# Kernel optimization log

Hardware: AMD Instinct MI355X
Metric: run time of the kernel (lower is better)

The kernel has to match this reference:

```python
import jax, jax.numpy as jnp
import numpy as np

B, S, D, H = 8, 1024, 1024, 16  # batch, seq (queries==keys), d_model, heads
DH = D // H


def setup_inputs() -> dict:
    key = jax.random.key(0)
    ks = jax.random.split(key, 7)
    return {
        "query": jax.random.normal(ks[0], (B, S, D), dtype=jnp.float32),
        "key": jax.random.normal(ks[1], (B, S, D), dtype=jnp.float32),
        "value": jax.random.normal(ks[2], (B, S, D), dtype=jnp.float32),
        "valid_len": jax.random.randint(ks[3], (B, S), 0, S, dtype=jnp.int32),
        "Wq": jax.random.normal(ks[4], (D, D), dtype=jnp.float32) / np.sqrt(D),
        "Wk": jax.random.normal(ks[5], (D, D), dtype=jnp.float32) / np.sqrt(D),
        "Wv": jax.random.normal(ks[6], (D, D), dtype=jnp.float32) / np.sqrt(D),
    }


def reference(query, key, value, valid_len, Wq, Wk, Wv):
    b, sq, _ = query.shape
    sk = key.shape[1]
    # projections (bias-free Linear), then split hidden into H contiguous chunks per head
    q = (query @ Wq).reshape(b, sq, H, DH)  # [B,Sq,H,dh]
    k = (key @ Wk).reshape(b, sk, H, DH)
    v = (value @ Wv).reshape(b, sk, H, DH)
    scale = 1.0 / jnp.sqrt(jnp.asarray(DH, dtype=q.dtype))
    scores = jnp.einsum("bqhd,bkhd->bhqk", q, k) * scale  # [B,H,Sq,Sk]
    # per-query mask (valid_len.dim()==2 path): key index < valid_len[b, q]
    col = jnp.arange(sk)
    mask = col[None, None, None, :] < valid_len[:, None, :, None]  # [B,1,Sq,Sk]
    scores = jnp.where(mask, scores, jnp.asarray(-1000.0, dtype=scores.dtype))
    prob = jax.nn.softmax(scores, axis=-1)
    out = jnp.einsum("bhqk,bkhd->bqhd", prob, v)  # [B,Sq,H,dh]
    return out.reshape(b, sq, D)
```

## Files before the change

kernel.cpp:

```cpp
#include <hip/hip_runtime.h>
#include <hip/hip_bf16.h>
#include <stdint.h>


#define B_  8
#define S_  1024
#define D_  1024
#define H_  16
#define DH_ 64

typedef short bf16x8 __attribute__((ext_vector_type(8)));
typedef float f32x4  __attribute__((ext_vector_type(4)));
typedef unsigned short u16;
typedef uint32_t u32;
typedef u16 u16x8 __attribute__((ext_vector_type(8)));
typedef u16 u16x4 __attribute__((ext_vector_type(4)));

#define MASKVAL  (-1442.6950408889634f)
#define QSCALE   (0.18033688011112042f)

union U4 { u32 u[4]; bf16x8 v; };

__device__ __forceinline__ u16 f2bf(float f) {
    union { float f; uint32_t u; } v; v.f = f;
    uint32_t u = v.u;
    return (u16)((u + 0x7FFFu + ((u >> 16) & 1u)) >> 16);
}

__device__ __forceinline__ u32 cvtpk(float lo, float hi) {
    u32 r;
    asm("v_cvt_pk_bf16_f32 %0, %1, %2" : "=v"(r) : "v"(lo), "v"(hi));
    return r;
}

__device__ __forceinline__ void gload16(const void* g, const void* l) {
    __builtin_amdgcn_global_load_lds(
        (const __attribute__((address_space(1))) void*)g,
        (__attribute__((address_space(3))) void*)l, 16, 0, 0);
}

__global__ void transpose_w3_kernel(const float* __restrict__ Wq, const float* __restrict__ Wk,
                                    const float* __restrict__ Wv, u16* __restrict__ Wts) {
    __shared__ u16 tile[32 * 33];
    const int z = blockIdx.z;
    const float* W = (z == 0) ? Wq : (z == 1) ? Wk : Wv;
    u16* Wt = Wts + (size_t)z * D_ * D_;
    int k0 = blockIdx.y * 32, n0 = blockIdx.x * 32;
    int t = threadIdx.x;
    int c = t & 31;
    for (int p = 0; p < 4; ++p) {
        int r = p * 8 + (t >> 5);
        tile[r * 33 + c] = f2bf(W[(size_t)(k0 + r) * D_ + n0 + c]);
    }
    __syncthreads();
    int rn = t >> 3, c4 = t & 7;
    u16x4 v;
    for (int j = 0; j < 4; ++j) v[j] = tile[(c4 * 4 + j) * 33 + rn];
    *(u16x4*)(Wt + (size_t)(n0 + rn) * D_ + k0 + c4 * 4) = v;
}

__global__ __launch_bounds__(1024) void sort_vlen_kernel(const int* __restrict__ vlen,
                                                         int* __restrict__ qidx) {
    __shared__ u32 sk[1024];
    const int b = blockIdx.x, t = threadIdx.x;
    int k = vlen[b * S_ + t];
    u32 key = (k == 0) ? (u32)S_ : (u32)k;
    sk[t] = (key << 10) | (u32)t;
    __syncthreads();
    for (int sz = 2; sz <= 1024; sz <<= 1) {
        for (int st = sz >> 1; st > 0; st >>= 1) {
            int j = t ^ st;
            if (j > t) {
                u32 a = sk[t], c = sk[j];
                bool des = (t & sz) != 0;
                if ((a > c) != des) { sk[t] = c; sk[j] = a; }
            }
            __syncthreads();
        }
    }
    qidx[b * S_ + t] = (int)(sk[t] & 1023u);
}

__global__ __launch_bounds__(256) void gemm_qkv_kernel(const float* __restrict__ Aq,
                                                       const float* __restrict__ Ak,
                                                       const float* __restrict__ Av,
                                                       const u16* __restrict__ wts,
                                                       u16* __restrict__ qb, u16* __restrict__ kb,
                                                       u16* __restrict__ vb) {
    __shared__ float lds_a[2][128 * 32];
    __shared__ u16  lds_b[2][128 * 32];
    const int zy = blockIdx.y;
    const int z = zy >> 3;
    const float* A = (z == 0) ? Aq : (z == 1) ? Ak : Av;
    const u16* Bt = wts + (size_t)z * D_ * D_;
    u16* C = (z == 0) ? qb : (z == 1) ? kb : vb;
    const float cmul = (z == 0) ? QSCALE : 1.0f;

    const int t = threadIdx.x, w = t >> 6, l = t & 63;
    const int m0 = blockIdx.x * 128, n0 = (zy & 7) * 128;
    const int wr = w >> 1, wc = w & 1;
    const int l15 = l & 15, l4 = l >> 4;
    f32x4 acc[4][4] = {};

    auto stage = [&](int buf, int kt) {
        int k0 = kt * 32;
        #pragma unroll
        for (int i = 0; i < 4; ++i) {
            int c = i * 256 + t;
            int row = c >> 3, xs = (c & 7) ^ (row & 7);
            gload16(A + (size_t)(m0 + row) * D_ + k0 + xs * 4, &lds_a[buf][c * 4]);
        }
        #pragma unroll
        for (int i = 0; i < 2; ++i) {
            int c = i * 256 + t;
            int row = c >> 2, x = c & 3;
            gload16(Bt + (size_t)(n0 + row) * D_ + k0 + x * 8, &lds_b[buf][c * 8]);
        }
    };

    stage(0, 0);
    __syncthreads();
    int buf = 0;
    for (int kt = 0; kt < 32; ++kt) {
        if (kt + 1 < 32) stage(buf ^ 1, kt + 1);
        bf16x8 af[4], bfr[4];
        #pragma unroll
        for (int mi = 0; mi < 4; ++mi) {
            int r = wr * 64 + mi * 16 + l15;
            int c0 = (l4 * 2) ^ (r & 7), c1 = (l4 * 2 + 1) ^ (r & 7);
            float4 fa0 = *(const float4*)&lds_a[buf][r * 32 + c0 * 4];
            float4 fa1 = *(const float4*)&lds_a[buf][r * 32 + c1 * 4];
            U4 d;
            d.u[0] = cvtpk(fa0.x, fa0.y); d.u[1] = cvtpk(fa0.z, fa0.w);
            d.u[2] = cvtpk(fa1.x, fa1.y); d.u[3] = cvtpk(fa1.z, fa1.w);
            af[mi] = d.v;
        }
        #pragma unroll
        for (int ni = 0; ni < 4; ++ni)
            bfr[ni] = *(const bf16x8*)&lds_b[buf][(wc * 64 + ni * 16 + l15) * 32 + l4 * 8];
        #pragma unroll
        for (int mi = 0; mi < 4; ++mi)
            #pragma unroll
            for (int ni = 0; ni < 4; ++ni)
                acc[mi][ni] = __builtin_amdgcn_mfma_f32_16x16x32_bf16(af[mi], bfr[ni], acc[mi][ni], 0, 0, 0);
        __syncthreads();
        buf ^= 1;
    }
    #pragma unroll
    for (int mi = 0; mi < 4; ++mi)
        #pragma unroll
        for (int ni = 0; ni < 4; ++ni)
            #pragma unroll
            for (int r = 0; r < 4; ++r) {
                int m = m0 + wr * 64 + mi * 16 + l4 * 4 + r;
                int n = n0 + wc * 64 + ni * 16 + l15;
                C[(size_t)m * D_ + n] = f2bf(acc[mi][ni][r] * cmul);
            }
}

__global__ void transpose_v_kernel(const u16* __restrict__ vb, u16* __restrict__ vt) {
    __shared__ u16 t2[64 * 72];
    int bid = blockIdx.x;
    int st = bid & 15, bh = bid >> 4;
    int b = bh >> 4, h = bh & 15;
    int t = threadIdx.x;
    for (int p = 0; p < 2; ++p) {
        int c = p * 256 + t, r = c >> 3, x = c & 7;
        u16x8 val = *(const u16x8*)&vb[((size_t)(b * S_ + st * 64 + r)) * D_ + h * 64 + x * 8];
        *(u16x8*)&t2[r * 72 + x * 8] = val;
    }
    __syncthreads();
    int d = t >> 2, kc = t & 3;
    u16x8 o0, o1;
    for (int j = 0; j < 8; ++j) o0[j] = t2[(kc * 16 + j) * 72 + d];
    for (int j = 0; j < 8; ++j) o1[j] = t2[(kc * 16 + 8 + j) * 72 + d];
    size_t obase = ((size_t)bh * 64 + d) * (size_t)S_ + st * 64 + kc * 16;
    *(u16x8*)&vt[obase] = o0;
    *(u16x8*)&vt[obase + 8] = o1;
}

__global__ __launch_bounds__(512) void attn_kernel(const u16* __restrict__ qb,
                                                   const u16* __restrict__ kb,
                                                   const u16* __restrict__ vt,
                                                   const int* __restrict__ vlen,
                                                   const int* __restrict__ qidx,
                                                   float* __restrict__ out) {
    __shared__ __align__(16) char smem_raw[34816];
    auto kv = [&](int buf, int which) -> u16* {
        return (u16*)(smem_raw + buf * 16384 + which * 8192);
    };

    const int t = threadIdx.x, w = t >> 6, l = t & 63;
    const int n = blockIdx.x;
    const int x = n & 7, j = n >> 3;
    const int bh = x + 8 * (j >> 2);
    const int p = j & 3;
    const int b = bh >> 4, h = bh & 15;
    const int l15 = l & 15, l4 = l >> 4;
    const bool lo32 = (l < 32);
    const bool rowe = ((l & 16) == 0);

    const u16* kbase = kb + ((size_t)(b * S_)) * D_ + h * 64;
    const u16* vbase = vt + ((size_t)bh * 64) * (size_t)S_;

    const int kr_s = t >> 3, x_s = (t & 7) ^ (kr_s & 7);
    auto stage = [&](int buf, int kt) {
        gload16(kbase + (size_t)(kt * 64 + kr_s) * D_ + x_s * 8, &kv(buf, 0)[t * 8]);
        gload16(vbase + (size_t)kr_s * S_ + kt * 64 + x_s * 8, &kv(buf, 1)[t * 8]);
    };

    auto redist = [&](u32 P, u32 Q, u32& oe, u32& oo) {
        u32 t0 = (u32)__shfl_xor((int)Q, 32, 64);
        u32 X  = lo32 ? P : t0;
        u32 uh = lo32 ? t0 : P;
        u32 Y  = (u32)__shfl_xor((int)uh, 32, 64);
        u32 t1 = (u32)__shfl_xor((int)Y, 16, 64);
        u32 t2 = (u32)__shfl_xor((int)X, 16, 64);
        oe = rowe ? X : t1;
        oo = rowe ? t2 : Y;
    };

    for (int jb = 0; jb < 2; ++jb) {
        const int qblk = (jb == 0) ? (7 - p) : p;
        const int q0 = qblk * 128;

        const int qi = qidx[b * S_ + q0 + w * 16 + l15];
        const u16* qptr = qb + ((size_t)(b * S_ + qi)) * D_ + h * 64 + l4 * 8;
        const bf16x8 bq0 = *(const bf16x8*)qptr;
        const bf16x8 bq1 = *(const bf16x8*)(qptr + 32);
        const int vlq = vlen[b * S_ + qi];

        int mk = vlen[b * S_ + qidx[b * S_ + q0 + 127]];
        if (mk == 0) mk = S_;
        const int nkt = (mk + 63) >> 6;

        float m = -3.0e38f, lsum = 0.f;
        f32x4 acc[4] = {};

        stage(0, 0);
        __syncthreads();

        int buf = 0;
        for (int kt = 0; kt < nkt; ++kt) {
            if (kt + 1 < nkt) stage(buf ^ 1, kt + 1);

            f32x4 sc[4];
            __builtin_amdgcn_s_setprio(1);
            #pragma unroll
            for (int nf = 0; nf < 4; ++nf) {
                int kr = nf * 16 + l15, swz = kr & 7;
                bf16x8 ak0 = *(const bf16x8*)&kv(buf, 0)[kr * 64 + ((l4 ^ swz) * 8)];
                bf16x8 ak1 = *(const bf16x8*)&kv(buf, 0)[kr * 64 + (((l4 + 4) ^ swz) * 8)];
                f32x4 s = {0.f, 0.f, 0.f, 0.f};
                s = __builtin_amdgcn_mfma_f32_16x16x32_bf16(ak0, bq0, s, 0, 0, 0);
                s = __builtin_amdgcn_mfma_f32_16x16x32_bf16(ak1, bq1, s, 0, 0, 0);
                sc[nf] = s;
            }
            __builtin_amdgcn_s_setprio(0);

            const int thr = vlq - kt * 64 - 4 * l4;
            float pv[16];
            float pm = -3.0e38f;
            #pragma unroll
            for (int nf = 0; nf < 4; ++nf)
                #pragma unroll
                for (int r = 0; r < 4; ++r) {
                    float y = ((nf * 16 + r) < thr) ? sc[nf][r] : MASKVAL;
                    pv[nf * 4 + r] = y;
                    pm = fmaxf(pm, y);
                }
            pm = fmaxf(pm, __shfl_xor(pm, 16, 64));
            pm = fmaxf(pm, __shfl_xor(pm, 32, 64));
            if (!__all(pm - m <= 8.0f)) {
                float mn = fmaxf(m, pm);
                float corr = __builtin_amdgcn_exp2f(m - mn);
                m = mn;
                lsum *= corr;
                #pragma unroll
                for (int df = 0; df < 4; ++df) acc[df] *= corr;
            }
            float rs = 0.f;
            #pragma unroll
            for (int i = 0; i < 16; ++i) {
                float e = __builtin_amdgcn_exp2f(pv[i] - m);
                pv[i] = e;
                rs += e;
            }
            rs += __shfl_xor(rs, 16, 64);
            rs += __shfl_xor(rs, 32, 64);
            lsum += rs;

            u32 pw[8];
            #pragma unroll
            for (int nf = 0; nf < 4; ++nf) {
                pw[2 * nf]     = cvtpk(pv[4 * nf + 0], pv[4 * nf + 1]);
                pw[2 * nf + 1] = cvtpk(pv[4 * nf + 2], pv[4 * nf + 3]);
            }
            U4 pb0, pb1;
            redist(pw[0], pw[2], pb0.u[0], pb0.u[2]);
            redist(pw[1], pw[3], pb0.u[1], pb0.u[3]);
            redist(pw[4], pw[6], pb1.u[0], pb1.u[2]);
            redist(pw[5], pw[7], pb1.u[1], pb1.u[3]);

            __builtin_amdgcn_s_setprio(1);
            #pragma unroll
            for (int df = 0; df < 4; ++df) {
                int vr = df * 16 + l15, swz = vr & 7;
                bf16x8 av0 = *(const bf16x8*)&kv(buf, 1)[vr * 64 + ((l4 ^ swz) * 8)];
                bf16x8 av1 = *(const bf16x8*)&kv(buf, 1)[vr * 64 + (((l4 + 4) ^ swz) * 8)];
                acc[df] = __builtin_amdgcn_mfma_f32_16x16x32_bf16(av0, pb0.v, acc[df], 0, 0, 0);
                acc[df] = __builtin_amdgcn_mfma_f32_16x16x32_bf16(av1, pb1.v, acc[df], 0, 0, 0);
            }
            __builtin_amdgcn_s_setprio(0);

            __syncthreads();
            buf ^= 1;
        }

        const float inv = 1.0f / lsum;
        __syncthreads();
        float* ep = (float*)smem_raw;
        #pragma unroll
        for (int df = 0; df < 4; ++df)
            #pragma unroll
            for (int r = 0; r < 4; ++r)
                ep[w * 1088 + l15 * 68 + df * 16 + 4 * l4 + r] = acc[df][r] * inv;
        __syncthreads();
        #pragma unroll
        for (int rr = 0; rr < 4; ++rr) {
            int row = l4 * 4 + rr;
            int qi2 = qidx[b * S_ + q0 + w * 16 + row];
            float4 vv = *(float4*)&ep[w * 1088 + row * 68 + l15 * 4];
            *(float4*)&out[((size_t)(b * S_ + qi2)) * D_ + h * 64 + l15 * 4] = vv;
        }
        __syncthreads();
    }
}

extern "C" void kernel_launch(void* const* d_in, const int* in_sizes, int n_in,
                              void* d_out, int out_size, void* d_ws, size_t ws_size,
                              hipStream_t stream) {
    const float* query = (const float*)d_in[0];
    const float* key   = (const float*)d_in[1];
    const float* value = (const float*)d_in[2];
    const int*   vlen  = (const int*)d_in[3];
    const float* Wq    = (const float*)d_in[4];
    const float* Wk    = (const float*)d_in[5];
    const float* Wv    = (const float*)d_in[6];
    float* out = (float*)d_out;

    char* ws = (char*)d_ws;
    const size_t MB = 1024 * 1024;
    const size_t TSZ = (size_t)B_ * S_ * D_ * 2;
    u16* wts = (u16*)(ws);
    u16* vt  = (u16*)(ws + 6 * MB);
    u16* qb  = (u16*)(ws + 6 * MB + TSZ);
    u16* kb  = (u16*)(ws + 6 * MB + 2 * TSZ);
    u16* vb  = (u16*)(ws + 6 * MB + 3 * TSZ);
    int* qidx = (int*)(ws + 6 * MB + 4 * TSZ);

    dim3 blk(256);

    transpose_w3_kernel<<<dim3(32, 32, 3), blk, 0, stream>>>(Wq, Wk, Wv, wts);
    sort_vlen_kernel<<<B_, dim3(1024), 0, stream>>>(vlen, qidx);

    gemm_qkv_kernel<<<dim3(64, 24), blk, 0, stream>>>(query, key, value, wts, qb, kb, vb);

    transpose_v_kernel<<<B_ * H_ * (S_ / 64), blk, 0, stream>>>(vb, vt);

    attn_kernel<<<dim3(512), dim3(512), 0, stream>>>(qb, kb, vt, vlen, qidx, out);
}
```

Before: 154.3 us.

## Skip per-wave key tiles past max valid length; use permlane32 swaps

Each wave computes the maximum valid length over its 16 queries and skips the QK, softmax and PV work for key tiles beyond it, while the block still stages tiles for other waves. Tiles that are fully unmasked take a fast path with no mask selects. Cross-half shuffles in the reductions and the P redistribution are replaced with v_permlane32_swap instead of ds_bpermute-based shuffles. Skipped waves still join the barriers, so this removes compute but not synchronization or load traffic.

Result: faster. 150.3 us (-2.6%).

```diff
diff --git a/kernel.cpp b/kernel.cpp
--- a/kernel.cpp
+++ b/kernel.cpp
@@ -37,6 +37,19 @@
     __builtin_amdgcn_global_load_lds(
         (const __attribute__((address_space(1))) void*)g,
         (__attribute__((address_space(3))) void*)l, 16, 0, 0);
+}
+
+__device__ __forceinline__ float xor32max(float v) {
+    float a = v, b = v;
+    asm volatile("" : "+v"(b));
+    asm("v_permlane32_swap_b32 %0, %1" : "+v"(a), "+v"(b));
+    return fmaxf(a, b);
+}
+__device__ __forceinline__ float xor32add(float v) {
+    float a = v, b = v;
+    asm volatile("" : "+v"(b));
+    asm("v_permlane32_swap_b32 %0, %1" : "+v"(a), "+v"(b));
+    return a + b;
 }
 
 __global__ void transpose_w3_kernel(const float* __restrict__ Wq, const float* __restrict__ Wk,
@@ -197,7 +210,6 @@
     const int p = j & 3;
     const int b = bh >> 4, h = bh & 15;
     const int l15 = l & 15, l4 = l >> 4;
-    const bool lo32 = (l < 32);
     const bool rowe = ((l & 16) == 0);
 
     const u16* kbase = kb + ((size_t)(b * S_)) * D_ + h * 64;
@@ -210,10 +222,8 @@
     };
 
     auto redist = [&](u32 P, u32 Q, u32& oe, u32& oo) {
-        u32 t0 = (u32)__shfl_xor((int)Q, 32, 64);
-        u32 X  = lo32 ? P : t0;
-        u32 uh = lo32 ? t0 : P;
-        u32 Y  = (u32)__shfl_xor((int)uh, 32, 64);
+        u32 X = P, Y = Q;
+        asm("v_permlane32_swap_b32 %0, %1" : "+v"(X), "+v"(Y));
         u32 t1 = (u32)__shfl_xor((int)Y, 16, 64);
         u32 t2 = (u32)__shfl_xor((int)X, 16, 64);
         oe = rowe ? X : t1;
@@ -234,6 +244,15 @@
         if (mk == 0) mk = S_;
         const int nkt = (mk + 63) >> 6;
 
+        int vm = (vlq == 0) ? S_ : vlq;
+        {
+            int s1 = __shfl_xor(vm, 1, 64);  vm = vm > s1 ? vm : s1;
+            int s2 = __shfl_xor(vm, 2, 64);  vm = vm > s2 ? vm : s2;
+            int s4 = __shfl_xor(vm, 4, 64);  vm = vm > s4 ? vm : s4;
+            int s8 = __shfl_xor(vm, 8, 64);  vm = vm > s8 ? vm : s8;
+        }
+        const int nktw = (vm + 63) >> 6;
+
         float m = -3.0e38f, lsum = 0.f;
         f32x4 acc[4] = {};
 
@@ -244,74 +263,87 @@
         for (int kt = 0; kt < nkt; ++kt) {
             if (kt + 1 < nkt) stage(buf ^ 1, kt + 1);
 
-            f32x4 sc[4];
-            __builtin_amdgcn_s_setprio(1);
-            #pragma unroll
-            for (int nf = 0; nf < 4; ++nf) {
-                int kr = nf * 16 + l15, swz = kr & 7;
-                bf16x8 ak0 = *(const bf16x8*)&kv(buf, 0)[kr * 64 + ((l4 ^ swz) * 8)];
-                bf16x8 ak1 = *(const bf16x8*)&kv(buf, 0)[kr * 64 + (((l4 + 4) ^ swz) * 8)];
-                f32x4 s = {0.f, 0.f, 0.f, 0.f};
-                s = __builtin_amdgcn_mfma_f32_16x16x32_bf16(ak0, bq0, s, 0, 0, 0);
-                s = __builtin_amdgcn_mfma_f32_16x16x32_bf16(ak1, bq1, s, 0, 0, 0);
-                sc[nf] = s;
+            if (kt < nktw) {
+                f32x4 sc[4];
+                __builtin_amdgcn_s_setprio(1);
+                #pragma unroll
+                for (int nf = 0; nf < 4; ++nf) {
+                    int kr = nf * 16 + l15, swz = kr & 7;
+                    bf16x8 ak0 = *(const bf16x8*)&kv(buf, 0)[kr * 64 + ((l4 ^ swz) * 8)];
+                    bf16x8 ak1 = *(const bf16x8*)&kv(buf, 0)[kr * 64 + (((l4 + 4) ^ swz) * 8)];
+                    f32x4 s = {0.f, 0.f, 0.f, 0.f};
+                    s = __builtin_amdgcn_mfma_f32_16x16x32_bf16(ak0, bq0, s, 0, 0, 0);
+                    s = __builtin_amdgcn_mfma_f32_16x16x32_bf16(ak1, bq1, s, 0, 0, 0);
+                    sc[nf] = s;
+                }
+                __builtin_amdgcn_s_setprio(0);
+
+                const int thr = vlq - kt * 64 - 4 * l4;
+                float pv[16];
+                float pm = -3.0e38f;
+                if (__all(thr >= 52)) {
+                    #pragma unroll
+                    for (int nf = 0; nf < 4; ++nf)
+                        #pragma unroll
+                        for (int r = 0; r < 4; ++r) {
+                            float y = sc[nf][r];
+                            pv[nf * 4 + r] = y;
+                            pm = fmaxf(pm, y);
+                        }
+                } else {
+                    #pragma unroll
+                    for (int nf = 0; nf < 4; ++nf)
+                        #pragma unroll
+                        for (int r = 0; r < 4; ++r) {
+                            float y = ((nf * 16 + r) < thr) ? sc[nf][r] : MASKVAL;
+                            pv[nf * 4 + r] = y;
+                            pm = fmaxf(pm, y);
+                        }
+                }
+                pm = fmaxf(pm, __shfl_xor(pm, 16, 64));
+                pm = xor32max(pm);
+                if (!__all(pm - m <= 8.0f)) {
+                    float mn = fmaxf(m, pm);
+                    float corr = __builtin_amdgcn_exp2f(m - mn);
+                    m = mn;
+                    lsum *= corr;
+                    #pragma unroll
+                    for (int df = 0; df < 4; ++df) acc[df] *= corr;
+                }
+                float rs = 0.f;
+                #pragma unroll
+                for (int i = 0; i < 16; ++i) {
+                    float e = __builtin_amdgcn_exp2f(pv[i] - m);
+                    pv[i] = e;
+                    rs += e;
+                }
+                rs += __shfl_xor(rs, 16, 64);
+                rs = xor32add(rs);
+                lsum += rs;
+
+                u32 pw[8];
+                #pragma unroll
+                for (int nf = 0; nf < 4; ++nf) {
+                    pw[2 * nf]     = cvtpk(pv[4 * nf + 0], pv[4 * nf + 1]);
+                    pw[2 * nf + 1] = cvtpk(pv[4 * nf + 2], pv[4 * nf + 3]);
+                }
+                U4 pb0, pb1;
+                redist(pw[0], pw[2], pb0.u[0], pb0.u[2]);
+                redist(pw[1], pw[3], pb0.u[1], pb0.u[3]);
+                redist(pw[4], pw[6], pb1.u[0], pb1.u[2]);
+                redist(pw[5], pw[7], pb1.u[1], pb1.u[3]);
+
+                __builtin_amdgcn_s_setprio(1);
+                #pragma unroll
+                for (int df = 0; df < 4; ++df) {
+                    int vr = df * 16 + l15, swz = vr & 7;
+                    bf16x8 av0 = *(const bf16x8*)&kv(buf, 1)[vr * 64 + ((l4 ^ swz) * 8)];
+                    bf16x8 av1 = *(const bf16x8*)&kv(buf, 1)[vr * 64 + (((l4 + 4) ^ swz) * 8)];
+                    acc[df] = __builtin_amdgcn_mfma_f32_16x16x32_bf16(av0, pb0.v, acc[df], 0, 0, 0);
+                    acc[df] = __builtin_amdgcn_mfma_f32_16x16x32_bf16(av1, pb1.v, acc[df], 0, 0, 0);
+                }
+                __builtin_amdgcn_s_setprio(0);
             }
-            __builtin_amdgcn_s_setprio(0);
-
-            const int thr = vlq - kt * 64 - 4 * l4;
-            float pv[16];
-            float pm = -3.0e38f;
-            #pragma unroll
-            for (int nf = 0; nf < 4; ++nf)
-                #pragma unroll
-                for (int r = 0; r < 4; ++r) {
-                    float y = ((nf * 16 + r) < thr) ? sc[nf][r] : MASKVAL;
-                    pv[nf * 4 + r] = y;
-                    pm = fmaxf(pm, y);
-                }
-            pm = fmaxf(pm, __shfl_xor(pm, 16, 64));
-            pm = fmaxf(pm, __shfl_xor(pm, 32, 64));
-            if (!__all(pm - m <= 8.0f)) {
-                float mn = fmaxf(m, pm);
-                float corr = __builtin_amdgcn_exp2f(m - mn);
-                m = mn;
-                lsum *= corr;
-                #pragma unroll
-                for (int df = 0; df < 4; ++df) acc[df] *= corr;
-            }
-            float rs = 0.f;
-            #pragma unroll
-            for (int i = 0; i < 16; ++i) {
-                float e = __builtin_amdgcn_exp2f(pv[i] - m);
-                pv[i] = e;
-                rs += e;
-            }
-            rs += __shfl_xor(rs, 16, 64);
-            rs += __shfl_xor(rs, 32, 64);
-            lsum += rs;
-
-            u32 pw[8];
-            #pragma unroll
-            for (int nf = 0; nf < 4; ++nf) {
-                pw[2 * nf]     = cvtpk(pv[4 * nf + 0], pv[4 * nf + 1]);
-                pw[2 * nf + 1] = cvtpk(pv[4 * nf + 2], pv[4 * nf + 3]);
-            }
-            U4 pb0, pb1;
-            redist(pw[0], pw[2], pb0.u[0], pb0.u[2]);
-            redist(pw[1], pw[3], pb0.u[1], pb0.u[3]);
-            redist(pw[4], pw[6], pb1.u[0], pb1.u[2]);
-            redist(pw[5], pw[7], pb1.u[1], pb1.u[3]);
-
-            __builtin_amdgcn_s_setprio(1);
-            #pragma unroll
-            for (int df = 0; df < 4; ++df) {
-                int vr = df * 16 + l15, swz = vr & 7;
-                bf16x8 av0 = *(const bf16x8*)&kv(buf, 1)[vr * 64 + ((l4 ^ swz) * 8)];
-                bf16x8 av1 = *(const bf16x8*)&kv(buf, 1)[vr * 64 + (((l4 + 4) ^ swz) * 8)];
-                acc[df] = __builtin_amdgcn_mfma_f32_16x16x32_bf16(av0, pb0.v, acc[df], 0, 0, 0);
-                acc[df] = __builtin_amdgcn_mfma_f32_16x16x32_bf16(av1, pb1.v, acc[df], 0, 0, 0);
-            }
-            __builtin_amdgcn_s_setprio(0);
 
             __syncthreads();
             buf ^= 1;
```
